# Optimization experiments

Measured on AMD Instinct MI355X. Metric: run time of the kernel, lower is better.

## Reference

```python
import jax, jax.numpy as jnp
import numpy as np

N, D, F, C = 50000, 16, 128, 40  # nodes, fixed neighbor count, feat dim (hidden/2), classes


def _w(k, shape, fan_in):
    return jax.random.normal(k, shape, jnp.float32) / np.float32(np.sqrt(fan_in))


def setup_inputs() -> dict:
    key = jax.random.key(0)
    ks = jax.random.split(key, 8)
    z = lambda *s: jnp.zeros(s, jnp.float32)
    inp = {
        "x": jax.random.normal(ks[0], (N, F), jnp.float32),
        "edge_src": jax.random.randint(ks[1], (N, D), 0, N),  # dst is implicitly arange(N), sorted
        "W1": _w(ks[2], (F, F), F), "b1": z(F),
        "W2": _w(ks[3], (3 * F, F), F), "b2": z(3 * F),
        "W3": _w(ks[4], (F, 3 * F), 3 * F), "b3": z(F),
    }
    for i, (kb, oc) in (("1", (ks[5], F)), ("2", (ks[6], C))):
        pass  # placeholder (loop built below)
    for i, kb, oc in (("1", ks[5], F), ("2", ks[6], C)):
        kk = jax.random.split(kb, 5)
        inp["Wp" + i] = _w(kk[0], (F, F), F); inp["bp" + i] = z(F)
        inp["Wih" + i] = _w(kk[1], (4 * F, F), F)
        inp["Whh" + i] = _w(kk[2], (4 * F, F), F)
        inp["bih" + i] = z(4 * F); inp["bhh" + i] = z(4 * F)
        inp["Wl" + i] = _w(kk[3], (oc, F), F); inp["bl" + i] = z(oc)
        inp["Wr" + i] = _w(kk[4], (oc, F), F)
    return inp


def lstm_last(seq, Wih, Whh, bih, bhh):
    """seq: [N, T, F] -> final hidden state [N, H] (torch LSTM gate order i,f,g,o)."""
    Hh = Whh.shape[1]
    b = bih + bhh

    def step(carry, xt):
        h, c = carry
        g = xt @ Wih.T + h @ Whh.T + b
        i, f, gg, o = jnp.split(g, 4, axis=-1)
        c = jax.nn.sigmoid(f) * c + jax.nn.sigmoid(i) * jnp.tanh(gg)
        h = jax.nn.sigmoid(o) * jnp.tanh(c)
        return (h, c), None

    h0 = jnp.zeros((seq.shape[0], Hh), seq.dtype)
    (h, _), _ = jax.lax.scan(step, (h0, h0), jnp.swapaxes(seq, 0, 1))
    return h


def sage_conv_lstm(x, edge_src, Wp, bp, Wih, Whh, bih, bhh, Wl, bl, Wr):
    """PyG SAGEConv(aggr='lstm', project=True) with fixed per-node degree D."""
    xp = jax.nn.relu(x @ Wp.T + bp)           # project source features
    msgs = xp[edge_src]                        # [N, D, F] neighbor gather (sorted by dst)
    aggr = lstm_last(msgs, Wih, Whh, bih, bhh)  # LSTM over each neighborhood
    return aggr @ Wl.T + bl + x @ Wr.T         # lin_l(aggr) + lin_r(root)


def reference(x, edge_src, W1, b1, W2, b2, W3, b3,
              Wp1, bp1, Wih1, Whh1, bih1, bhh1, Wl1, bl1, Wr1,
              Wp2, bp2, Wih2, Whh2, bih2, bhh2, Wl2, bl2, Wr2):
    # Dead MLP branch: original forward computes it then overwrites h with conv1(x, ...)
    h = jax.nn.relu(x @ W1.T + b1)
    h = jax.nn.relu(h @ W2.T + b2)
    h = jax.nn.relu(h @ W3.T + b3)
    del h
    h = jax.nn.relu(sage_conv_lstm(x, edge_src, Wp1, bp1, Wih1, Whh1, bih1, bhh1, Wl1, bl1, Wr1))
    return sage_conv_lstm(h, edge_src, Wp2, bp2, Wih2, Whh2, bih2, bhh2, Wl2, bl2, Wr2)
```

## Files before the change

kernel.cpp:

```cpp
#include <hip/hip_runtime.h>
#include <hip/hip_bf16.h>


typedef __hip_bfloat16 bf16;
typedef __attribute__((ext_vector_type(8))) short short8;
typedef __attribute__((ext_vector_type(4))) short short4v;
typedef __attribute__((ext_vector_type(4))) float floatx4;
typedef __attribute__((ext_vector_type(4))) float float4v;

#define LOG2E 1.4426950408889634f
#define TWOL  2.8853900817779268f

__device__ __forceinline__ float bf2f(bf16 v) { return __bfloat162float(v); }
__device__ __forceinline__ bf16  f2bf(float v) { return __float2bfloat16(v); }
__device__ __forceinline__ float bfs2f(short s) {
    union { float f; unsigned u; } v; v.u = ((unsigned)(unsigned short)s) << 16; return v.f;
}
__device__ __forceinline__ short f2bfs(float v) {
    bf16 b = __float2bfloat16(v); return *(short*)&b;
}

__device__ __forceinline__ float ex2(float x) {
#if __has_builtin(__builtin_amdgcn_exp2f)
    return __builtin_amdgcn_exp2f(x);
#else
    return exp2f(x);
#endif
}

__device__ __forceinline__ float cell(float i_, float f_, float g_, float o_, float& c) {
    float ei = ex2(-i_), ef = ex2(-f_), eg = ex2(g_), eo = ex2(-o_);
    float A = (1.f + ei) * (eg + 1.f);
    float B = 1.f + ef;
    float cn = fmaf(c, A, fmaf(eg, TWOL, -TWOL) * B) * __builtin_amdgcn_rcpf(A * B);
    c = cn;
    float ec = ex2(cn);
    return (ec - 1.f) * __builtin_amdgcn_rcpf((ec + 1.f) * (1.f + eo));
}

__device__ __forceinline__ int ydecode(int p) {
    int pw = (p >> 6) & 7, pq = (p >> 4) & 3, pg = (p >> 2) & 3, pr = p & 3;
    return pg * 128 + pw * 16 + pq * 4 + pr;
}

__device__ __forceinline__ void dma2(const bf16* gp, void* lp0, void* lp1) {
    __builtin_amdgcn_global_load_lds(
        (const __attribute__((address_space(1))) void*)gp,
        (__attribute__((address_space(3))) void*)lp0, 16, 0, 0);
    __builtin_amdgcn_global_load_lds(
        (const __attribute__((address_space(1))) void*)(gp + 32),
        (__attribute__((address_space(3))) void*)lp1, 16, 0, 0);
}

struct Cvt { const void* src; const void* src2; bf16* dst; int n; int mode; };
struct CvtAll { Cvt t[17]; };

__global__ void convert_inputs(CvtAll ca, int* __restrict__ flag) {
    __shared__ int sflag;
    {
        const unsigned short* xb = (const unsigned short*)ca.t[0].src;
        int cnt = 0;
        for (int i = threadIdx.x; i < 1024; i += blockDim.x) {
            int e = (xb[i] >> 7) & 0xFF;
            cnt += (e >= 0xC8);
        }
        if (threadIdx.x == 0) sflag = 0;
        __syncthreads();
        if (cnt) atomicAdd(&sflag, cnt);
        __syncthreads();
    }
    const bool isf32 = (sflag >= 16);
    if (blockIdx.x == 0 && threadIdx.x == 0) *flag = isf32 ? 1 : 0;

    const int stride = gridDim.x * blockDim.x;
    const int tid0 = blockIdx.x * blockDim.x + threadIdx.x;
#pragma unroll 1
    for (int k = 0; k < 17; k++) {
        const int n = ca.t[k].n, mode = ca.t[k].mode;
        if (mode == 3) {
            const float* a32 = (const float*)ca.t[k].src;
            const float* b32 = (const float*)ca.t[k].src2;
            const short* a16 = (const short*)ca.t[k].src;
            const short* b16 = (const short*)ca.t[k].src2;
            float* df = (float*)ca.t[k].dst;
            for (int i = tid0; i < n; i += stride) {
                int yd = ydecode(i);
                float va = isf32 ? a32[yd] : bfs2f(a16[yd]);
                float vb = isf32 ? b32[yd] : bfs2f(b16[yd]);
                float m = ((((unsigned)i >> 2) & 3) == 2) ? TWOL : LOG2E;
                df[i] = (va + vb) * m;
            }
            continue;
        }
        const int n8 = n >> 3;
        bf16* d = ca.t[k].dst;
        for (int i = tid0; i < n8; i += stride) {
            int si = i;
            float m = 1.f;
            bool scaled = false;
            if (mode == 1) {
                m = ((((unsigned)i >> 11) & 3) == 2) ? TWOL : LOG2E; scaled = true;
            } else if (mode == 2) {
                int row = i >> 4;
                si = ydecode(row) * 16 + (i & 15);
                m = ((((unsigned)row >> 2) & 3) == 2) ? TWOL : LOG2E; scaled = true;
            }
            short8 ov;
            if (isf32) {
                const float4v* sp = (const float4v*)ca.t[k].src;
                float4v a = sp[2 * si], b = sp[2 * si + 1];
#pragma unroll
                for (int j = 0; j < 4; j++) {
                    ov[j]     = f2bfs(a[j] * m);
                    ov[4 + j] = f2bfs(b[j] * m);
                }
            } else {
                short8 sv = ((const short8*)ca.t[k].src)[si];
                if (scaled) {
#pragma unroll
                    for (int j = 0; j < 8; j++) ov[j] = f2bfs(bfs2f(sv[j]) * m);
                } else ov = sv;
            }
            ((short8*)d)[i] = ov;
        }
        if (mode == 0)
            for (int i = (n8 << 3) + tid0; i < n; i += stride) {
                float v = isf32 ? ((const float*)ca.t[k].src)[i]
                                : bfs2f(((const short*)ca.t[k].src)[i]);
                d[i] = f2bf(v);
            }
    }
}

__global__ __launch_bounds__(256, 2) void fused_xp_y(
    const bf16* __restrict__ X, const bf16* __restrict__ Wp, const bf16* __restrict__ bp,
    const bf16* __restrict__ Wihp, const float* __restrict__ bsum,
    bf16* __restrict__ Yout, int N)
{
    __shared__ bf16 T[64][136];
    const int tid = threadIdx.x;
    const int w = tid >> 6, l = tid & 63, q = l >> 4, lid = l & 15;
    const int rowbase = blockIdx.x * 64;

    int arow = rowbase + w * 16 + lid;
    if (arow >= N) arow = N - 1;

    floatx4 acc[8];
    short8 bfrag[8][4];
    float bvv[8];

#pragma unroll
    for (int ct = 0; ct < 8; ct++) acc[ct] = (floatx4)(0.f);
#pragma unroll
    for (int ct = 0; ct < 8; ct++) {
        int j = lid * 8 + ct;
        bvv[ct] = bf2f(bp[j]);
#pragma unroll
        for (int kt = 0; kt < 4; kt++)
            bfrag[ct][kt] = *(const short8*)(Wp + (size_t)j * 128 + kt * 32 + q * 8);
    }
#pragma unroll
    for (int kt = 0; kt < 4; kt++) {
        short8 af = *(const short8*)(X + (size_t)arow * 128 + kt * 32 + q * 8);
#pragma unroll
        for (int ct = 0; ct < 8; ct++)
            acc[ct] = __builtin_amdgcn_mfma_f32_16x16x32_bf16(af, bfrag[ct][kt], acc[ct], 0, 0, 0);
    }
#pragma unroll
    for (int r = 0; r < 4; r++) {
        short8 ov;
#pragma unroll
        for (int ct = 0; ct < 8; ct++)
            ov[ct] = f2bfs(fmaxf(acc[ct][r] + bvv[ct], 0.f));
        *(short8*)&T[w * 16 + q * 4 + r][lid * 8] = ov;
    }
    __syncthreads();

#pragma unroll 1
    for (int cc = 0; cc < 4; cc++) {
#pragma unroll
        for (int ct = 0; ct < 8; ct++) {
            int pos = cc * 128 + lid * 8 + ct;
            bvv[ct] = bsum[pos];
#pragma unroll
            for (int kt = 0; kt < 4; kt++)
                bfrag[ct][kt] = *(const short8*)(Wihp + (size_t)pos * 128 + kt * 32 + q * 8);
        }
#pragma unroll
        for (int ct = 0; ct < 8; ct++) acc[ct] = (floatx4)(0.f);
#pragma unroll
        for (int kt = 0; kt < 4; kt++) {
            short8 af = *(const short8*)&T[w * 16 + lid][kt * 32 + q * 8];
#pragma unroll
            for (int ct = 0; ct < 8; ct++)
                acc[ct] = __builtin_amdgcn_mfma_f32_16x16x32_bf16(af, bfrag[ct][kt], acc[ct], 0, 0, 0);
        }
#pragma unroll
        for (int r = 0; r < 4; r++) {
            int row = rowbase + w * 16 + q * 4 + r;
            if (row < N) {
                short8 ov;
#pragma unroll
                for (int ct = 0; ct < 8; ct++)
                    ov[ct] = f2bfs(acc[ct][r] + bvv[ct]);
                *(short8*)(Yout + (size_t)row * 512 + cc * 128 + lid * 8) = ov;
            }
        }
    }
}

__global__ __launch_bounds__(256, 2) void fused_lin_xp_y(
    const bf16* __restrict__ aggr, const bf16* __restrict__ Wl, const bf16* __restrict__ bl,
    const bf16* __restrict__ X, const bf16* __restrict__ Wr,
    bf16* __restrict__ h1out,
    const bf16* __restrict__ Wp2, const bf16* __restrict__ bp2,
    const bf16* __restrict__ Wihp2, const float* __restrict__ bsum2,
    bf16* __restrict__ Yout, int N)
{
    __shared__ bf16 T1[64][136];
    __shared__ bf16 T2[64][136];
    const int tid = threadIdx.x;
    const int w = tid >> 6, l = tid & 63, q = l >> 4, lid = l & 15;
    const int rowbase = blockIdx.x * 64;

    int arow = rowbase + w * 16 + lid;
    if (arow >= N) arow = N - 1;

    floatx4 acc[8];
    short8 bfrag[8][4];
    float bvv[8];

#pragma unroll
    for (int ct = 0; ct < 8; ct++) acc[ct] = (floatx4)(0.f);
#pragma unroll
    for (int ct = 0; ct < 8; ct++) {
        int j = lid * 8 + ct;
        bvv[ct] = bf2f(bl[j]);
#pragma unroll
        for (int kt = 0; kt < 4; kt++)
            bfrag[ct][kt] = *(const short8*)(Wl + (size_t)j * 128 + kt * 32 + q * 8);
    }
#pragma unroll
    for (int kt = 0; kt < 4; kt++) {
        short8 af = *(const short8*)(aggr + (size_t)arow * 128 + kt * 32 + q * 8);
#pragma unroll
        for (int ct = 0; ct < 8; ct++)
            acc[ct] = __builtin_amdgcn_mfma_f32_16x16x32_bf16(af, bfrag[ct][kt], acc[ct], 0, 0, 0);
    }
#pragma unroll
    for (int ct = 0; ct < 8; ct++) {
        int j = lid * 8 + ct;
#pragma unroll
        for (int kt = 0; kt < 4; kt++)
            bfrag[ct][kt] = *(const short8*)(Wr + (size_t)j * 128 + kt * 32 + q * 8);
    }
#pragma unroll
    for (int kt = 0; kt < 4; kt++) {
        short8 af = *(const short8*)(X + (size_t)arow * 128 + kt * 32 + q * 8);
#pragma unroll
        for (int ct = 0; ct < 8; ct++)
            acc[ct] = __builtin_amdgcn_mfma_f32_16x16x32_bf16(af, bfrag[ct][kt], acc[ct], 0, 0, 0);
    }
#pragma unroll
    for (int r = 0; r < 4; r++) {
        short8 ov;
#pragma unroll
        for (int ct = 0; ct < 8; ct++)
            ov[ct] = f2bfs(fmaxf(acc[ct][r] + bvv[ct], 0.f));
        int rl = w * 16 + q * 4 + r;
        *(short8*)&T1[rl][lid * 8] = ov;
        int row = rowbase + rl;
        if (row < N) *(short8*)(h1out + (size_t)row * 128 + lid * 8) = ov;
    }
    __syncthreads();

#pragma unroll
    for (int ct = 0; ct < 8; ct++) {
        int j = lid * 8 + ct;
        bvv[ct] = bf2f(bp2[j]);
#pragma unroll
        for (int kt = 0; kt < 4; kt++)
            bfrag[ct][kt] = *(const short8*)(Wp2 + (size_t)j * 128 + kt * 32 + q * 8);
    }
#pragma unroll
    for (int ct = 0; ct < 8; ct++) acc[ct] = (floatx4)(0.f);
#pragma unroll
    for (int kt = 0; kt < 4; kt++) {
        short8 af = *(const short8*)&T1[w * 16 + lid][kt * 32 + q * 8];
#pragma unroll
        for (int ct = 0; ct < 8; ct++)
            acc[ct] = __builtin_amdgcn_mfma_f32_16x16x32_bf16(af, bfrag[ct][kt], acc[ct], 0, 0, 0);
    }
#pragma unroll
    for (int r = 0; r < 4; r++) {
        short8 ov;
#pragma unroll
        for (int ct = 0; ct < 8; ct++)
            ov[ct] = f2bfs(fmaxf(acc[ct][r] + bvv[ct], 0.f));
        *(short8*)&T2[w * 16 + q * 4 + r][lid * 8] = ov;
    }
    __syncthreads();

#pragma unroll 1
    for (int cc = 0; cc < 4; cc++) {
#pragma unroll
        for (int ct = 0; ct < 8; ct++) {
            int pos = cc * 128 + lid * 8 + ct;
            bvv[ct] = bsum2[pos];
#pragma unroll
            for (int kt = 0; kt < 4; kt++)
                bfrag[ct][kt] = *(const short8*)(Wihp2 + (size_t)pos * 128 + kt * 32 + q * 8);
        }
#pragma unroll
        for (int ct = 0; ct < 8; ct++) acc[ct] = (floatx4)(0.f);
#pragma unroll
        for (int kt = 0; kt < 4; kt++) {
            short8 af = *(const short8*)&T2[w * 16 + lid][kt * 32 + q * 8];
#pragma unroll
            for (int ct = 0; ct < 8; ct++)
                acc[ct] = __builtin_amdgcn_mfma_f32_16x16x32_bf16(af, bfrag[ct][kt], acc[ct], 0, 0, 0);
        }
#pragma unroll
        for (int r = 0; r < 4; r++) {
            int row = rowbase + w * 16 + q * 4 + r;
            if (row < N) {
                short8 ov;
#pragma unroll
                for (int ct = 0; ct < 8; ct++)
                    ov[ct] = f2bfs(acc[ct][r] + bvv[ct]);
                *(short8*)(Yout + (size_t)row * 512 + cc * 128 + lid * 8) = ov;
            }
        }
    }
}

template <int EPI>
__global__ __launch_bounds__(512, 4) void lstm_aggr(
    const bf16* __restrict__ Y,
    const int* __restrict__ esrc,
    const bf16* __restrict__ Whh,
    bf16* __restrict__ aggr,
    int N,
    const bf16* __restrict__ Wl2, const bf16* __restrict__ bl2,
    const bf16* __restrict__ Wr2, const bf16* __restrict__ h1,
    void* __restrict__ outp, const int* __restrict__ oflag)
{
    __shared__ alignas(16) short stage[2][8][1024];
    __shared__ alignas(16) bf16 hb[2][16][136];
    __shared__ int srcl[16][16];

    const int tid = threadIdx.x;
    const int w = tid >> 6, l = tid & 63, q = l >> 4, lid = l & 15;
    const int nodebase = blockIdx.x * 16;

    if (tid < 256) {
        int node = tid >> 4, t = tid & 15;
        srcl[t][node] = esrc[(size_t)(nodebase + node) * 16 + t];
    }

    short8 wf[4][4];
#pragma unroll
    for (int g = 0; g < 4; g++) {
        int gc = g * 128 + 16 * w + lid;
#pragma unroll
        for (int kt = 0; kt < 4; kt++)
            wf[g][kt] = *(const short8*)(Whh + (size_t)gc * 128 + kt * 32 + q * 8);
    }

    float c[4];
#pragma unroll
    for (int r = 0; r < 4; r++) c[r] = 0.f;

    const int laneoff = w * 64 + q * 8;

    __syncthreads();

    {
        int s0 = srcl[0][lid];
        dma2(Y + (size_t)s0 * 512 + laneoff, &stage[0][w][0], &stage[0][w][512]);
        int s1 = srcl[1][lid];
        dma2(Y + (size_t)s1 * 512 + laneoff, &stage[1][w][0], &stage[1][w][512]);
    }

#pragma unroll 2
    for (int t = 0; t < 16; t++) {
        const int cb = t & 1;

        if (t == 15) asm volatile("s_waitcnt vmcnt(0)" ::: "memory");
        else         asm volatile("s_waitcnt vmcnt(2)" ::: "memory");

        int snext = (t < 14) ? srcl[t + 2][lid] : 0;

        floatx4 acc[4];
        {
            const short* wbuf = &stage[cb][w][0];
            short8 y0 = *(const short8*)&wbuf[q * 256 + lid * 8];
            short8 y1 = *(const short8*)&wbuf[q * 256 + 128 + lid * 8];
#pragma unroll
            for (int g = 0; g < 2; g++)
#pragma unroll
                for (int r = 0; r < 4; r++) {
                    acc[g][r]     = bfs2f(y0[g * 4 + r]);
                    acc[2 + g][r] = bfs2f(y1[g * 4 + r]);
                }
        }

        if (t) {
#pragma unroll
            for (int kt = 0; kt < 4; kt++) {
                short8 bh = *(const short8*)&hb[cb][lid][kt * 32 + q * 8];
#pragma unroll
                for (int g = 0; g < 4; g++)
                    acc[g] = __builtin_amdgcn_mfma_f32_16x16x32_bf16(wf[g][kt], bh, acc[g], 0, 0, 0);
            }
        }

        {
            short4v hv;
#pragma unroll
            for (int r = 0; r < 4; r++)
                hv[r] = f2bfs(cell(acc[0][r], acc[1][r], acc[2][r], acc[3][r], c[r]));
            if (t < 15) *(short4v*)&hb[cb ^ 1][lid][16 * w + 4 * q] = hv;
            else if (EPI == 0)
                *(short4v*)(aggr + (size_t)(nodebase + lid) * 128 + 16 * w + 4 * q) = hv;
            else
                *(short4v*)&hb[0][lid][16 * w + 4 * q] = hv;
        }

        if (t < 15) {
            asm volatile("s_waitcnt lgkmcnt(0)" ::: "memory");
            if (t < 14)
                dma2(Y + (size_t)snext * 512 + laneoff, &stage[cb][w][0], &stage[cb][w][512]);
            __builtin_amdgcn_s_barrier();
        }
    }

    if constexpr (EPI == 1) {
        asm volatile("s_waitcnt lgkmcnt(0)" ::: "memory");
        __builtin_amdgcn_s_barrier();
        if (w < 3) {
            int j = w * 16 + lid;
            int jc = j < 40 ? j : 39;
            short8 blf[4], brf[4];
#pragma unroll
            for (int kt = 0; kt < 4; kt++) {
                blf[kt] = *(const short8*)(Wl2 + (size_t)jc * 128 + kt * 32 + q * 8);
                brf[kt] = *(const short8*)(Wr2 + (size_t)jc * 128 + kt * 32 + q * 8);
            }
            floatx4 o = (floatx4)(0.f);
#pragma unroll
            for (int kt = 0; kt < 4; kt++) {
                short8 ah = *(const short8*)&hb[0][lid][kt * 32 + q * 8];
                o = __builtin_amdgcn_mfma_f32_16x16x32_bf16(ah, blf[kt], o, 0, 0, 0);
            }
#pragma unroll
            for (int kt = 0; kt < 4; kt++) {
                short8 a1 = *(const short8*)(h1 + (size_t)(nodebase + lid) * 128 + kt * 32 + q * 8);
                o = __builtin_amdgcn_mfma_f32_16x16x32_bf16(a1, brf[kt], o, 0, 0, 0);
            }
            float bv = bf2f(bl2[jc]);
            bool of32 = (*oflag != 0);
            if (j < 40) {
#pragma unroll
                for (int r = 0; r < 4; r++) {
                    int node = nodebase + q * 4 + r;
                    float v = o[r] + bv;
                    size_t idx = (size_t)node * 40 + j;
                    if (of32) ((float*)outp)[idx] = v;
                    else      ((bf16*)outp)[idx]  = f2bf(v);
                }
            }
        }
    }
}

extern "C" void kernel_launch(void* const* d_in, const int* in_sizes, int n_in,
                              void* d_out, int out_size, void* d_ws, size_t ws_size,
                              hipStream_t stream)
{
    const int N = 50000;
    const int* es = (const int*)d_in[1];
    char* ws = (char*)d_ws;

    struct Ent { int di; int di2; int mode; int n; };
    Ent ents[17] = {
        {0,  -1, 0, 0},
        {8,  -1, 0, 0}, {9,  -1, 0, 0},
        {10, -1, 2, 0}, {11, -1, 1, 0},
        {12, 13, 3, 0},
        {14, -1, 0, 0}, {15, -1, 0, 0}, {16, -1, 0, 0},
        {17, -1, 0, 0}, {18, -1, 0, 0},
        {19, -1, 2, 0}, {20, -1, 1, 0},
        {21, 22, 3, 0},
        {23, -1, 0, 0}, {24, -1, 0, 0}, {25, -1, 0, 0},
    };
    bf16* conv[17];
    size_t off = 0;
    CvtAll ca;
    for (int k = 0; k < 17; k++) {
        conv[k] = (bf16*)ws + off;
        int n = in_sizes[ents[k].di];
        ca.t[k].src  = d_in[ents[k].di];
        ca.t[k].src2 = ents[k].di2 >= 0 ? d_in[ents[k].di2] : nullptr;
        ca.t[k].dst  = conv[k];
        ca.t[k].n    = n;
        ca.t[k].mode = ents[k].mode;
        size_t elems = (ents[k].mode == 3) ? (size_t)n * 2 : (size_t)n;
        off += (elems + 63) & ~(size_t)63;
    }
    int* flag  = (int*)(ws + ((size_t)15 << 20));
    bf16* aggr = (bf16*)(ws + ((size_t)16 << 20));
    bf16* Y    = (bf16*)(ws + ((size_t)30 << 20));
    bf16* h1   = (bf16*)(ws + ((size_t)84 << 20));

    const bf16 *xc   = conv[0];
    const bf16 *Wp1  = conv[1],  *bp1 = conv[2];
    const bf16 *Wihp1 = conv[3], *Whh1 = conv[4];
    const float *bsum1 = (const float*)conv[5];
    const bf16 *Wl1 = conv[6], *bl1 = conv[7], *Wr1 = conv[8];
    const bf16 *Wp2 = conv[9], *bp2 = conv[10];
    const bf16 *Wihp2 = conv[11], *Whh2 = conv[12];
    const float *bsum2 = (const float*)conv[13];
    const bf16 *Wl2 = conv[14], *bl2 = conv[15], *Wr2 = conv[16];

    dim3 blk(256);
    const int gx = (N + 63) / 64;
    const int gl = N / 16;

    convert_inputs<<<dim3(1024), blk, 0, stream>>>(ca, flag);

    fused_xp_y<<<dim3(gx), blk, 0, stream>>>(xc, Wp1, bp1, Wihp1, bsum1, Y, N);
    lstm_aggr<0><<<dim3(gl), dim3(512), 0, stream>>>(
        Y, es, Whh1, aggr, N, nullptr, nullptr, nullptr, nullptr, nullptr, nullptr);

    fused_lin_xp_y<<<dim3(gx), blk, 0, stream>>>(
        aggr, Wl1, bl1, xc, Wr1, h1, Wp2, bp2, Wihp2, bsum2, Y, N);

    lstm_aggr<1><<<dim3(gl), dim3(512), 0, stream>>>(
        Y, es, Whh2, aggr, N, Wl2, bl2, Wr2, h1, d_out, flag);
}
```

Before: 655.5 us.

## Keep Wih fragments resident per wave and prefetch h1 into LDS for epilogue

In the projection kernels, each wave now owns one 128-column gate chunk and loads its Wih fragments and bias once, then loops over the four 16-row tiles. Before, every wave reloaded fragments for all four chunks. This cuts the weight reloads from global memory. In the LSTM epilogue, the h1 root rows are DMA'd into the now-idle stage buffer during the last step, and the Wl2/Wr2 fragments are loaded before the barrier, so these global loads overlap with the final recurrence step. The tradeoff is a different store pattern (each wave writes strided rows) and reuse of the stage LDS, which depends on careful waitcnt ordering.

```diff
diff --git a/kernel.cpp b/kernel.cpp
--- a/kernel.cpp
+++ b/kernel.cpp
@@ -43,13 +43,15 @@
     return pg * 128 + pw * 16 + pq * 4 + pr;
 }
 
-__device__ __forceinline__ void dma2(const bf16* gp, void* lp0, void* lp1) {
+__device__ __forceinline__ void dma1(const bf16* gp, void* lp) {
     __builtin_amdgcn_global_load_lds(
         (const __attribute__((address_space(1))) void*)gp,
-        (__attribute__((address_space(3))) void*)lp0, 16, 0, 0);
-    __builtin_amdgcn_global_load_lds(
-        (const __attribute__((address_space(1))) void*)(gp + 32),
-        (__attribute__((address_space(3))) void*)lp1, 16, 0, 0);
+        (__attribute__((address_space(3))) void*)lp, 16, 0, 0);
+}
+
+__device__ __forceinline__ void dma2(const bf16* gp, void* lp0, void* lp1) {
+    dma1(gp, lp0);
+    dma1(gp + 32, lp1);
 }
 
 struct Cvt { const void* src; const void* src2; bf16* dst; int n; int mode; };
@@ -176,34 +178,34 @@
     }
     __syncthreads();
 
+#pragma unroll
+    for (int ct = 0; ct < 8; ct++) {
+        int pos = w * 128 + lid * 8 + ct;
+        bvv[ct] = bsum[pos];
+#pragma unroll
+        for (int kt = 0; kt < 4; kt++)
+            bfrag[ct][kt] = *(const short8*)(Wihp + (size_t)pos * 128 + kt * 32 + q * 8);
+    }
 #pragma unroll 1
-    for (int cc = 0; cc < 4; cc++) {
-#pragma unroll
-        for (int ct = 0; ct < 8; ct++) {
-            int pos = cc * 128 + lid * 8 + ct;
-            bvv[ct] = bsum[pos];
-#pragma unroll
-            for (int kt = 0; kt < 4; kt++)
-                bfrag[ct][kt] = *(const short8*)(Wihp + (size_t)pos * 128 + kt * 32 + q * 8);
-        }
+    for (int rt = 0; rt < 4; rt++) {
 #pragma unroll
         for (int ct = 0; ct < 8; ct++) acc[ct] = (floatx4)(0.f);
 #pragma unroll
         for (int kt = 0; kt < 4; kt++) {
-            short8 af = *(const short8*)&T[w * 16 + lid][kt * 32 + q * 8];
+            short8 af = *(const short8*)&T[rt * 16 + lid][kt * 32 + q * 8];
 #pragma unroll
             for (int ct = 0; ct < 8; ct++)
                 acc[ct] = __builtin_amdgcn_mfma_f32_16x16x32_bf16(af, bfrag[ct][kt], acc[ct], 0, 0, 0);
         }
 #pragma unroll
         for (int r = 0; r < 4; r++) {
-            int row = rowbase + w * 16 + q * 4 + r;
+            int row = rowbase + rt * 16 + q * 4 + r;
             if (row < N) {
                 short8 ov;
 #pragma unroll
                 for (int ct = 0; ct < 8; ct++)
                     ov[ct] = f2bfs(acc[ct][r] + bvv[ct]);
-                *(short8*)(Yout + (size_t)row * 512 + cc * 128 + lid * 8) = ov;
+                *(short8*)(Yout + (size_t)row * 512 + w * 128 + lid * 8) = ov;
             }
         }
     }
@@ -301,34 +303,34 @@
     }
     __syncthreads();
 
+#pragma unroll
+    for (int ct = 0; ct < 8; ct++) {
+        int pos = w * 128 + lid * 8 + ct;
+        bvv[ct] = bsum2[pos];
+#pragma unroll
+        for (int kt = 0; kt < 4; kt++)
+            bfrag[ct][kt] = *(const short8*)(Wihp2 + (size_t)pos * 128 + kt * 32 + q * 8);
+    }
 #pragma unroll 1
-    for (int cc = 0; cc < 4; cc++) {
-#pragma unroll
-        for (int ct = 0; ct < 8; ct++) {
-            int pos = cc * 128 + lid * 8 + ct;
-            bvv[ct] = bsum2[pos];
-#pragma unroll
-            for (int kt = 0; kt < 4; kt++)
-                bfrag[ct][kt] = *(const short8*)(Wihp2 + (size_t)pos * 128 + kt * 32 + q * 8);
-        }
+    for (int rt = 0; rt < 4; rt++) {
 #pragma unroll
         for (int ct = 0; ct < 8; ct++) acc[ct] = (floatx4)(0.f);
 #pragma unroll
         for (int kt = 0; kt < 4; kt++) {
-            short8 af = *(const short8*)&T2[w * 16 + lid][kt * 32 + q * 8];
+            short8 af = *(const short8*)&T2[rt * 16 + lid][kt * 32 + q * 8];
 #pragma unroll
             for (int ct = 0; ct < 8; ct++)
                 acc[ct] = __builtin_amdgcn_mfma_f32_16x16x32_bf16(af, bfrag[ct][kt], acc[ct], 0, 0, 0);
         }
 #pragma unroll
         for (int r = 0; r < 4; r++) {
-            int row = rowbase + w * 16 + q * 4 + r;
+            int row = rowbase + rt * 16 + q * 4 + r;
             if (row < N) {
                 short8 ov;
 #pragma unroll
                 for (int ct = 0; ct < 8; ct++)
                     ov[ct] = f2bfs(acc[ct][r] + bvv[ct]);
-                *(short8*)(Yout + (size_t)row * 512 + cc * 128 + lid * 8) = ov;
+                *(short8*)(Yout + (size_t)row * 512 + w * 128 + lid * 8) = ov;
             }
         }
     }
@@ -389,6 +391,11 @@
         if (t == 15) asm volatile("s_waitcnt vmcnt(0)" ::: "memory");
         else         asm volatile("s_waitcnt vmcnt(2)" ::: "memory");
 
+        if (EPI == 1 && t == 15 && w < 4) {
+            const bf16* gp = h1 + (size_t)(nodebase + w * 4 + q) * 128 + lid * 8;
+            dma1(gp, (char*)&stage[0][0][0] + (tid << 4 & ~1023 ? 0 : 0) + w * 1024);
+        }
+
         int snext = (t < 14) ? srcl[t + 2][lid] : 0;
 
         floatx4 acc[4];
@@ -436,17 +443,21 @@
     }
 
     if constexpr (EPI == 1) {
+        asm volatile("s_waitcnt vmcnt(0)" ::: "memory");
+        short8 blf[4], brf[4];
+        int j = w * 16 + lid;
+        int jc = j < 40 ? j : 39;
+        if (w < 3) {
+#pragma unroll
+            for (int kt = 0; kt < 4; kt++) {
+                blf[kt] = *(const short8*)(Wl2 + (size_t)jc * 128 + kt * 32 + q * 8);
+                brf[kt] = *(const short8*)(Wr2 + (size_t)jc * 128 + kt * 32 + q * 8);
+            }
+        }
         asm volatile("s_waitcnt lgkmcnt(0)" ::: "memory");
         __builtin_amdgcn_s_barrier();
         if (w < 3) {
-            int j = w * 16 + lid;
-            int jc = j < 40 ? j : 39;
-            short8 blf[4], brf[4];
-#pragma unroll
-            for (int kt = 0; kt < 4; kt++) {
-                blf[kt] = *(const short8*)(Wl2 + (size_t)jc * 128 + kt * 32 + q * 8);
-                brf[kt] = *(const short8*)(Wr2 + (size_t)jc * 128 + kt * 32 + q * 8);
-            }
+            const short* h1b = &stage[0][0][0];
             floatx4 o = (floatx4)(0.f);
 #pragma unroll
             for (int kt = 0; kt < 4; kt++) {
@@ -455,7 +466,7 @@
             }
 #pragma unroll
             for (int kt = 0; kt < 4; kt++) {
-                short8 a1 = *(const short8*)(h1 + (size_t)(nodebase + lid) * 128 + kt * 32 + q * 8);
+                short8 a1 = *(const short8*)&h1b[lid * 128 + kt * 32 + q * 8];
                 o = __builtin_amdgcn_mfma_f32_16x16x32_bf16(a1, brf[kt], o, 0, 0, 0);
             }
             float bv = bf2f(bl2[jc]);
@@ -482,17 +493,17 @@
     const int* es = (const int*)d_in[1];
     char* ws = (char*)d_ws;
 
-    struct Ent { int di; int di2; int mode; int n; };
+    struct Ent { int di; int di2; int mode; };
     Ent ents[17] = {
-        {0,  -1, 0, 0},
-        {8,  -1, 0, 0}, {9,  -1, 0, 0},
-        {10, -1, 2, 0}, {11, -1, 1, 0},
-        {12, 13, 3, 0},
-        {14, -1, 0, 0}, {15, -1, 0, 0}, {16, -1, 0, 0},
-        {17, -1, 0, 0}, {18, -1, 0, 0},
-        {19, -1, 2, 0}, {20, -1, 1, 0},
-        {21, 22, 3, 0},
-        {23, -1, 0, 0}, {24, -1, 0, 0}, {25, -1, 0, 0},
+        {0,  -1, 0},
+        {8,  -1, 0}, {9,  -1, 0},
+        {10, -1, 2}, {11, -1, 1},
+        {12, 13, 3},
+        {14, -1, 0}, {15, -1, 0}, {16, -1, 0},
+        {17, -1, 0}, {18, -1, 0},
+        {19, -1, 2}, {20, -1, 1},
+        {21, 22, 3},
+        {23, -1, 0}, {24, -1, 0}, {25, -1, 0},
     };
     bf16* conv[17];
     size_t off = 0;
```

New measurement: 575.4 us. 1.14x faster.
